# Performance work log

Measured on AMD Instinct MI355X. Metric: run time of the kernel, lower is better.

## Reference

```python
import jax, jax.numpy as jnp
import numpy as np

NUM_HEADS = 16
HIDDEN = 1024
HEAD_DIM = HIDDEN // NUM_HEADS
B, S, D = 2, 2048, 1024


def setup_inputs() -> dict:
    key = jax.random.key(0)
    ks = jax.random.split(key, 7)
    scale = 1.0 / np.sqrt(D)
    return {
        "query": jax.random.normal(ks[0], (B, S, D), dtype=jnp.float32),
        "key": jax.random.normal(ks[1], (B, S, D), dtype=jnp.float32),
        "value": jax.random.normal(ks[2], (B, S, D), dtype=jnp.float32),
        "Wk_w": jax.random.normal(ks[3], (HIDDEN, D), dtype=jnp.float32) * scale,
        "Wk_b": jax.random.normal(ks[4], (HIDDEN,), dtype=jnp.float32) * scale,
        "Wv_w": jax.random.normal(ks[5], (HIDDEN, D), dtype=jnp.float32) * scale,
        "Wv_b": jax.random.normal(ks[6], (HIDDEN,), dtype=jnp.float32) * scale,
    }


def reference(query, key, value, Wk_w, Wk_b, Wv_w, Wv_b):
    # NOTE: in the original torch module, self.W_v is assigned twice, so the
    # SAME Linear (Wv) projects both key and value; Wk projects query.
    b, s, _ = query.shape

    def split_heads(x):  # [b,s,hidden] -> [b,h,s,hd]
        return x.reshape(b, s, NUM_HEADS, HEAD_DIM).transpose(0, 2, 1, 3)

    q = split_heads(query @ Wk_w.T + Wk_b)
    k = split_heads(key @ Wv_w.T + Wv_b)
    v = split_heads(value @ Wv_w.T + Wv_b)

    scores = jnp.einsum("bhqd,bhkd->bhqk", q, k) / jnp.sqrt(
        jnp.asarray(HEAD_DIM, dtype=q.dtype))
    probs = jax.nn.softmax(scores, axis=-1)
    out = jnp.einsum("bhqk,bhkd->bhqd", probs, v)
    return out.transpose(0, 2, 1, 3).reshape(b, s, NUM_HEADS * HEAD_DIM)
```

## Files before the change

kernel.cpp:

```cpp
#include <hip/hip_runtime.h>
#include <stdint.h>

typedef unsigned short u16;
typedef uint32_t u32;
typedef __bf16 bf16x8 __attribute__((ext_vector_type(8)));
typedef float f32x4 __attribute__((ext_vector_type(4)));
typedef u16 u16x4 __attribute__((ext_vector_type(4)));
typedef u16 u16x8 __attribute__((ext_vector_type(8)));

#define XQ_OFF 0ul
#define XK_OFF 4194304ul
#define XV_OFF 8388608ul
#define WK_OFF 12582912ul
#define WV_OFF 13631488ul
#define Q_OFF  14680064ul
#define K_OFF  18874368ul
#define V_OFF  23068672ul

#define SCQ 0.18033688011112042f

#if __has_builtin(__builtin_amdgcn_exp2f)
#define EXP2F(x) __builtin_amdgcn_exp2f(x)
#else
#define EXP2F(x) exp2f(x)
#endif

__device__ __forceinline__ u16 f2bf(float f) {
  u32 u = __float_as_uint(f);
  u32 r = (u + 0x7fffu + ((u >> 16) & 1u)) >> 16;
  return (u16)r;
}

__device__ __forceinline__ u32 pk2(float a, float b) {
  typedef __bf16 bf2_t __attribute__((ext_vector_type(2)));
  typedef float f2_t __attribute__((ext_vector_type(2)));
  f2_t v; v[0] = a; v[1] = b;
  bf2_t h = __builtin_convertvector(v, bf2_t);
  union { bf2_t h; u32 u; } cv; cv.h = h; return cv.u;
}

__device__ __forceinline__ void load_lds16(const void* g, void* l) {
  __builtin_amdgcn_global_load_lds(
      (const __attribute__((address_space(1))) u32*)g,
      (__attribute__((address_space(3))) u32*)l, 16, 0, 0);
}

__device__ __forceinline__ u32 swz(u32 L) {
  return L ^ (((L >> 7) & 1u) << 4) ^ (((L >> 10) & 3u) << 5);
}

__global__ __launch_bounds__(256) void cvt_tile_kernel(
    const float* __restrict__ xq, const float* __restrict__ xk,
    const float* __restrict__ xv, const float* __restrict__ wk,
    const float* __restrict__ wv, u16* __restrict__ ws) {
  __shared__ u16 tile[4096];
  const int bid = blockIdx.x;
  const float* src; size_t dstbase; int rt, ktp;
  if (bid < 3072) {
    int m = bid >> 10, loc = bid & 1023;
    src = (m == 0) ? xq : (m == 1) ? xk : xv;
    dstbase = (size_t)m * 4194304ul;
    rt = loc >> 4; ktp = loc & 15;
  } else {
    int r2 = bid - 3072;
    int m = r2 >> 8, loc = r2 & 255;
    src = m ? wv : wk;
    dstbase = WK_OFF + (size_t)m * 1048576ul;
    rt = loc >> 4; ktp = loc & 15;
  }
  const int t = threadIdx.x;
  const int row0 = t >> 4, c = t & 15;
  const int k = c * 4;
  const float* s = src + (size_t)(rt * 64 + row0) * 1024ul + ktp * 64 + k;
#pragma unroll
  for (int i = 0; i < 4; ++i) {
    float4 v = *(const float4*)(s + (size_t)i * 16384ul);
    int row = row0 + i * 16;
    u32* p = (u32*)(tile + ((k >> 5) * 2048 + ((k >> 3) & 3) * 512 + row * 8 + (k & 7)));
    p[0] = pk2(v.x, v.y);
    p[1] = pk2(v.z, v.w);
  }
  __syncthreads();
  u16* dst = ws + dstbase + (size_t)(rt * 32 + ktp * 2) * 2048ul;
#pragma unroll
  for (int so = 0; so < 4096; so += 2048)
    *(u16x8*)(dst + so + t * 8) = *(const u16x8*)(tile + so + t * 8);
}

__global__ __launch_bounds__(256, 3) void proj_kernel(u16* __restrict__ ws,
                                                      const float* __restrict__ bk,
                                                      const float* __restrict__ bv) {
  const int proj = blockIdx.z;
  const int mtile = blockIdx.x;
  const int ntile = blockIdx.y;
  const u16* A = ws + (size_t)proj * 4194304ul;
  const u16* Bw = ws + ((proj == 0) ? WK_OFF : WV_OFF);
  const float* bias = (proj == 0) ? bk : bv;
  u16* outQ = ws + Q_OFF;
  u16* outK = ws + K_OFF;
  u16* outV = ws + V_OFF;

  const int t = threadIdx.x;
  const int w = t >> 6, lane = t & 63;
  const int wm = w >> 1, wn = w & 1;
  const int g = lane >> 4, c = lane & 15;

  __shared__ __align__(16) u16 As[2][2][2048];
  __shared__ __align__(16) u16 Bs[2][2][2048];

  const u16* Ag = A + (size_t)(2 * mtile) * 65536ul;
  const u16* Bg = Bw + (size_t)(2 * ntile) * 65536ul;
  const u32 t8 = (u32)t * 8u;
  const u32 so = swz((u32)t * 16u) >> 1;

  u32 poff[4];
#pragma unroll
  for (int mt = 0; mt < 4; ++mt)
    poff[mt] = swz((u32)((g << 10) | ((mt * 16 + c) << 4))) >> 1;

#define PSTAGE(buf, kt)                                            \
  do {                                                             \
    const size_t ko = (size_t)(kt) * 2048ul + so;                  \
    load_lds16(Ag + ko, &As[buf][0][t8]);                          \
    load_lds16(Ag + 65536ul + ko, &As[buf][1][t8]);                \
    load_lds16(Bg + ko, &Bs[buf][0][t8]);                          \
    load_lds16(Bg + 65536ul + ko, &Bs[buf][1][t8]);                \
  } while (0)

  f32x4 acc[4][4];
#pragma unroll
  for (int mt = 0; mt < 4; ++mt)
#pragma unroll
    for (int nt = 0; nt < 4; ++nt) acc[mt][nt] = (f32x4){0.f, 0.f, 0.f, 0.f};

  PSTAGE(0, 0);
  __syncthreads();

#pragma unroll 1
  for (int kt = 0; kt < 32; ++kt) {
    const int cur = kt & 1;
    if (kt < 31) PSTAGE(cur ^ 1, kt + 1);
    const u16* Ap = As[cur][wm];
    const u16* Bp = Bs[cur][wn];
    bf16x8 af[4], bfv[4];
#pragma unroll
    for (int mt = 0; mt < 4; ++mt) af[mt] = *(const bf16x8*)(Ap + poff[mt]);
#pragma unroll
    for (int nt = 0; nt < 4; ++nt) bfv[nt] = *(const bf16x8*)(Bp + poff[nt]);
#pragma unroll
    for (int mt = 0; mt < 4; ++mt)
#pragma unroll
      for (int nt = 0; nt < 4; ++nt)
        acc[mt][nt] =
            __builtin_amdgcn_mfma_f32_16x16x32_bf16(af[mt], bfv[nt], acc[mt][nt], 0, 0, 0);
    __syncthreads();
  }
#undef PSTAGE

  const int m0 = mtile * 128 + wm * 64;
  const int n0 = ntile * 128 + wn * 64;
#pragma unroll
  for (int nt = 0; nt < 4; ++nt) {
    const int col = n0 + nt * 16 + c;
    const float bvv = bias[col];
    const int h = col >> 6, d = col & 63;
#pragma unroll
    for (int mt = 0; mt < 4; ++mt) {
      const int mbase = m0 + mt * 16 + g * 4;
      const int b = mbase >> 11;
      const int bh = b * 16 + h;
      const int s = mbase & 2047;
      if (proj == 2) {
        u16x4 pk;
#pragma unroll
        for (int r = 0; r < 4; ++r) pk[r] = f2bf(acc[mt][nt][r] + bvv);
        size_t idx = (size_t)bh * 131072ul + (size_t)(s >> 6) * 4096ul +
                     (size_t)((s & 63) >> 3) * 512ul + (size_t)d * 8ul + (size_t)(s & 7);
        *(u16x4*)(outV + idx) = pk;
      } else {
        u16* dst = (proj == 0) ? outQ : outK;
#pragma unroll
        for (int r = 0; r < 4; ++r) {
          const int m = mbase + r;
          const int s2 = m & 2047;
          float y = acc[mt][nt][r] + bvv;
          if (proj == 0) y *= SCQ;
          size_t idx;
          if (proj == 0)
            idx = (size_t)bh * 131072ul + (size_t)(s2 >> 7) * 8192ul + (size_t)(d >> 3) * 1024ul +
                  (size_t)(s2 & 127) * 8ul + (size_t)(d & 7);
          else
            idx = (size_t)bh * 131072ul + (size_t)(s2 >> 6) * 4096ul + (size_t)(d >> 3) * 512ul +
                  (size_t)(s2 & 63) * 8ul + (size_t)(d & 7);
          dst[idx] = f2bf(y);
        }
      }
    }
  }
}

__device__ __forceinline__ void attn_step(
    int jj, const u16* __restrict__ Kg, const u16* __restrict__ Vg,
    bf16x8 (&kf)[2][4], bf16x8 (&vcur)[2][4], bf16x8 (&vnxt)[2][4],
    const bf16x8 (&qf)[2][2], const bf16x8 onesf, f32x4 (&O)[2][4],
    f32x4 (&Lacc)[2], u16* __restrict__ Psw, int g, int c) {
  const int jn = (jj < 31) ? jj + 1 : 31;
  const u16* Vn = Vg + (size_t)jn * 4096ul;
#pragma unroll
  for (int ksh = 0; ksh < 2; ++ksh)
#pragma unroll
    for (int nt = 0; nt < 4; ++nt)
      vnxt[ksh][nt] = *(const bf16x8*)(Vn + (ksh * 4 + g) * 512 + (nt * 16 + c) * 8);

  f32x4 St[4][2];
#pragma unroll
  for (int mtk = 0; mtk < 4; ++mtk)
#pragma unroll
    for (int ntq = 0; ntq < 2; ++ntq) St[mtk][ntq] = (f32x4){0.f, 0.f, 0.f, 0.f};
  __builtin_amdgcn_s_setprio(1);
#pragma unroll
  for (int ks = 0; ks < 2; ++ks)
#pragma unroll
    for (int mtk = 0; mtk < 4; ++mtk)
#pragma unroll
      for (int ntq = 0; ntq < 2; ++ntq)
        St[mtk][ntq] =
            __builtin_amdgcn_mfma_f32_16x16x32_bf16(kf[ks][mtk], qf[ntq][ks], St[mtk][ntq], 0, 0, 0);
  __builtin_amdgcn_s_setprio(0);

  const u16* Kn = Kg + (size_t)jn * 4096ul;
#pragma unroll
  for (int ks = 0; ks < 2; ++ks)
#pragma unroll
    for (int mtk = 0; mtk < 4; ++mtk)
      kf[ks][mtk] = *(const bf16x8*)(Kn + (ks * 4 + g) * 512 + (mtk * 16 + c) * 8);

#pragma unroll
  for (int mtk = 0; mtk < 4; ++mtk)
#pragma unroll
    for (int ntq = 0; ntq < 2; ++ntq)
#pragma unroll
      for (int r = 0; r < 4; ++r) St[mtk][ntq][r] = EXP2F(St[mtk][ntq][r]);

#pragma unroll
  for (int ksh = 0; ksh < 2; ++ksh) {
#pragma unroll
    for (int ntq = 0; ntq < 2; ++ntq)
#pragma unroll
      for (int m2 = 0; m2 < 2; ++m2) {
        const int mtk = ksh * 2 + m2;
        u32 lo = pk2(St[mtk][ntq][0], St[mtk][ntq][1]);
        u32 hi = pk2(St[mtk][ntq][2], St[mtk][ntq][3]);
        u32* p = (u32*)(Psw + (ntq * 16 + c) * 40 + m2 * 16 + g * 4);
        p[0] = lo; p[1] = hi;
      }
    asm volatile("s_waitcnt lgkmcnt(0)" ::: "memory");
    bf16x8 pf[2];
#pragma unroll
    for (int mtq = 0; mtq < 2; ++mtq)
      pf[mtq] = *(const bf16x8*)(Psw + (mtq * 16 + c) * 40 + g * 8);
    __builtin_amdgcn_s_setprio(1);
#pragma unroll
    for (int mtq = 0; mtq < 2; ++mtq) {
      Lacc[mtq] = __builtin_amdgcn_mfma_f32_16x16x32_bf16(pf[mtq], onesf, Lacc[mtq], 0, 0, 0);
#pragma unroll
      for (int nt = 0; nt < 4; ++nt)
        O[mtq][nt] =
            __builtin_amdgcn_mfma_f32_16x16x32_bf16(pf[mtq], vcur[ksh][nt], O[mtq][nt], 0, 0, 0);
    }
    __builtin_amdgcn_s_setprio(0);
  }
}

__global__ __launch_bounds__(256, 2) void attn_kernel(const u16* __restrict__ ws,
                                                      float* __restrict__ out) {
  const int bh = blockIdx.x, qtile = blockIdx.y;
  const int b = bh >> 4, h = bh & 15;
  const int t = threadIdx.x, w = t >> 6, lane = t & 63, g = lane >> 4, c = lane & 15;

  __shared__ __align__(16) u16 Ps[4][1280];

  const u16* Qg = ws + Q_OFF + (size_t)bh * 131072ul + (size_t)qtile * 8192ul;
  const u16* Kg = ws + K_OFF + (size_t)bh * 131072ul;
  const u16* Vg = ws + V_OFF + (size_t)bh * 131072ul;

  bf16x8 qf[2][2];
#pragma unroll
  for (int ntq = 0; ntq < 2; ++ntq)
#pragma unroll
    for (int ks = 0; ks < 2; ++ks)
      qf[ntq][ks] = *(const bf16x8*)(Qg + (ks * 4 + g) * 1024 + (w * 32 + ntq * 16 + c) * 8);

  u16x8 ou;
#pragma unroll
  for (int i = 0; i < 8; ++i) ou[i] = (u16)0x3F80;
  union { u16x8 u; bf16x8 b; } ocv; ocv.u = ou;
  const bf16x8 onesf = ocv.b;

  f32x4 O[2][4], Lacc[2];
#pragma unroll
  for (int mtq = 0; mtq < 2; ++mtq) {
    Lacc[mtq] = (f32x4){0.f, 0.f, 0.f, 0.f};
#pragma unroll
    for (int nt = 0; nt < 4; ++nt) O[mtq][nt] = (f32x4){0.f, 0.f, 0.f, 0.f};
  }

  u16* Psw = Ps[w];

  bf16x8 kf[2][4];
#pragma unroll
  for (int ks = 0; ks < 2; ++ks)
#pragma unroll
    for (int mtk = 0; mtk < 4; ++mtk)
      kf[ks][mtk] = *(const bf16x8*)(Kg + (ks * 4 + g) * 512 + (mtk * 16 + c) * 8);
  bf16x8 vfA[2][4], vfB[2][4];
#pragma unroll
  for (int ksh = 0; ksh < 2; ++ksh)
#pragma unroll
    for (int nt = 0; nt < 4; ++nt)
      vfA[ksh][nt] = *(const bf16x8*)(Vg + (ksh * 4 + g) * 512 + (nt * 16 + c) * 8);

#pragma unroll 1
  for (int j2 = 0; j2 < 16; ++j2) {
    attn_step(2 * j2, Kg, Vg, kf, vfA, vfB, qf, onesf, O, Lacc, Psw, g, c);
    attn_step(2 * j2 + 1, Kg, Vg, kf, vfB, vfA, qf, onesf, O, Lacc, Psw, g, c);
  }

  const int q0 = qtile * 128 + w * 32;
#pragma unroll
  for (int mtq = 0; mtq < 2; ++mtq)
#pragma unroll
    for (int r = 0; r < 4; ++r) {
      const float inv = 1.0f / Lacc[mtq][r];
      const int q = q0 + mtq * 16 + g * 4 + r;
      float* rowp = out + (size_t)(b * 2048 + q) * 1024ul + h * 64;
#pragma unroll
      for (int nt = 0; nt < 4; ++nt) rowp[nt * 16 + c] = O[mtq][nt][r] * inv;
    }
}

extern "C" void kernel_launch(void* const* d_in, const int* in_sizes, int n_in,
                              void* d_out, int out_size, void* d_ws, size_t ws_size,
                              hipStream_t stream) {
  const float* q = (const float*)d_in[0];
  const float* k = (const float*)d_in[1];
  const float* v = (const float*)d_in[2];
  const float* wk = (const float*)d_in[3];
  const float* bk = (const float*)d_in[4];
  const float* wv = (const float*)d_in[5];
  const float* bv = (const float*)d_in[6];
  u16* ws = (u16*)d_ws;
  float* out = (float*)d_out;

  cvt_tile_kernel<<<3584, 256, 0, stream>>>(q, k, v, wk, wv, ws);
  proj_kernel<<<dim3(32, 8, 3), 256, 0, stream>>>(ws, bk, bv);
  attn_kernel<<<dim3(32, 16), 256, 0, stream>>>(ws, out);
}
```

Baseline: 180.3 us.

## Triple-buffer projection GEMM loads and stage Q/K epilogue through LDS

The projection GEMM moves from a double-buffered LDS pipeline to a three-stage ring. It prefetches two k-tiles ahead and uses an explicit vmcnt wait plus s_barrier in place of a full __syncthreads per iteration. The Q/K epilogue now writes bf16 results into per-warp LDS tiles first, then stores them to global memory as coalesced 16-byte vectors, replacing scattered 2-byte stores. This raises LDS use to 48KB per block, which may lower occupancy, and relies on hand-counted vmcnt values being correct.

```diff
diff --git a/kernel.cpp b/kernel.cpp
--- a/kernel.cpp
+++ b/kernel.cpp
@@ -105,8 +105,7 @@
   const int wm = w >> 1, wn = w & 1;
   const int g = lane >> 4, c = lane & 15;
 
-  __shared__ __align__(16) u16 As[2][2][2048];
-  __shared__ __align__(16) u16 Bs[2][2][2048];
+  __shared__ __align__(16) u16 smem[24576];
 
   const u16* Ag = A + (size_t)(2 * mtile) * 65536ul;
   const u16* Bg = Bw + (size_t)(2 * ntile) * 65536ul;
@@ -120,13 +119,29 @@
 
 #define PSTAGE(buf, kt)                                            \
   do {                                                             \
+    u16* bb = smem + (buf) * 8192;                                 \
     const size_t ko = (size_t)(kt) * 2048ul + so;                  \
-    load_lds16(Ag + ko, &As[buf][0][t8]);                          \
-    load_lds16(Ag + 65536ul + ko, &As[buf][1][t8]);                \
-    load_lds16(Bg + ko, &Bs[buf][0][t8]);                          \
-    load_lds16(Bg + 65536ul + ko, &Bs[buf][1][t8]);                \
+    load_lds16(Ag + ko, bb + t8);                                  \
+    load_lds16(Ag + 65536ul + ko, bb + 2048 + t8);                 \
+    load_lds16(Bg + ko, bb + 4096 + t8);                           \
+    load_lds16(Bg + 65536ul + ko, bb + 6144 + t8);                 \
   } while (0)
 
+#define PFRAGS_MFMA(buf)                                                        \
+  do {                                                                          \
+    const u16* Ap = smem + (buf) * 8192 + wm * 2048;                            \
+    const u16* Bp = smem + (buf) * 8192 + 4096 + wn * 2048;                     \
+    bf16x8 af[4], bfv[4];                                                       \
+    _Pragma("unroll") for (int mt = 0; mt < 4; ++mt)                            \
+        af[mt] = *(const bf16x8*)(Ap + poff[mt]);                               \
+    _Pragma("unroll") for (int nt = 0; nt < 4; ++nt)                            \
+        bfv[nt] = *(const bf16x8*)(Bp + poff[nt]);                              \
+    _Pragma("unroll") for (int mt = 0; mt < 4; ++mt)                            \
+        _Pragma("unroll") for (int nt = 0; nt < 4; ++nt)                        \
+            acc[mt][nt] = __builtin_amdgcn_mfma_f32_16x16x32_bf16(              \
+                af[mt], bfv[nt], acc[mt][nt], 0, 0, 0);                         \
+  } while (0)
+
   f32x4 acc[4][4];
 #pragma unroll
   for (int mt = 0; mt < 4; ++mt)
@@ -134,67 +149,75 @@
     for (int nt = 0; nt < 4; ++nt) acc[mt][nt] = (f32x4){0.f, 0.f, 0.f, 0.f};
 
   PSTAGE(0, 0);
-  __syncthreads();
-
+  PSTAGE(1, 1);
+
+  int cur = 0, stg = 2;
 #pragma unroll 1
-  for (int kt = 0; kt < 32; ++kt) {
-    const int cur = kt & 1;
-    if (kt < 31) PSTAGE(cur ^ 1, kt + 1);
-    const u16* Ap = As[cur][wm];
-    const u16* Bp = Bs[cur][wn];
-    bf16x8 af[4], bfv[4];
-#pragma unroll
-    for (int mt = 0; mt < 4; ++mt) af[mt] = *(const bf16x8*)(Ap + poff[mt]);
-#pragma unroll
-    for (int nt = 0; nt < 4; ++nt) bfv[nt] = *(const bf16x8*)(Bp + poff[nt]);
-#pragma unroll
-    for (int mt = 0; mt < 4; ++mt)
-#pragma unroll
-      for (int nt = 0; nt < 4; ++nt)
-        acc[mt][nt] =
-            __builtin_amdgcn_mfma_f32_16x16x32_bf16(af[mt], bfv[nt], acc[mt][nt], 0, 0, 0);
-    __syncthreads();
-  }
+  for (int kt = 0; kt < 31; ++kt) {
+    asm volatile("s_waitcnt vmcnt(4)\n\ts_barrier" ::: "memory");
+    if (kt < 30) PSTAGE(stg, kt + 2);
+    PFRAGS_MFMA(cur);
+    cur = (cur == 2) ? 0 : cur + 1;
+    stg = (stg == 2) ? 0 : stg + 1;
+  }
+  asm volatile("s_waitcnt vmcnt(0)\n\ts_barrier" ::: "memory");
+  PFRAGS_MFMA(cur);
 #undef PSTAGE
+#undef PFRAGS_MFMA
 
   const int m0 = mtile * 128 + wm * 64;
   const int n0 = ntile * 128 + wn * 64;
-#pragma unroll
-  for (int nt = 0; nt < 4; ++nt) {
-    const int col = n0 + nt * 16 + c;
-    const float bvv = bias[col];
-    const int h = col >> 6, d = col & 63;
-#pragma unroll
-    for (int mt = 0; mt < 4; ++mt) {
-      const int mbase = m0 + mt * 16 + g * 4;
-      const int b = mbase >> 11;
-      const int bh = b * 16 + h;
-      const int s = mbase & 2047;
-      if (proj == 2) {
+  if (proj == 2) {
+#pragma unroll
+    for (int nt = 0; nt < 4; ++nt) {
+      const int col = n0 + nt * 16 + c;
+      const float bvv = bias[col];
+      const int h = col >> 6, d = col & 63;
+#pragma unroll
+      for (int mt = 0; mt < 4; ++mt) {
+        const int mbase = m0 + mt * 16 + g * 4;
+        const int b = mbase >> 11;
+        const int bh = b * 16 + h;
+        const int s = mbase & 2047;
         u16x4 pk;
 #pragma unroll
         for (int r = 0; r < 4; ++r) pk[r] = f2bf(acc[mt][nt][r] + bvv);
         size_t idx = (size_t)bh * 131072ul + (size_t)(s >> 6) * 4096ul +
                      (size_t)((s & 63) >> 3) * 512ul + (size_t)d * 8ul + (size_t)(s & 7);
         *(u16x4*)(outV + idx) = pk;
-      } else {
-        u16* dst = (proj == 0) ? outQ : outK;
+      }
+    }
+  } else {
+    __syncthreads();
+    u16* Ew = smem + w * 4096;
+#pragma unroll
+    for (int nt = 0; nt < 4; ++nt) {
+      const int d = nt * 16 + c;
+      const float bvv = bias[n0 + nt * 16 + c];
+#pragma unroll
+      for (int mt = 0; mt < 4; ++mt) {
 #pragma unroll
         for (int r = 0; r < 4; ++r) {
-          const int m = mbase + r;
-          const int s2 = m & 2047;
+          const int srow = mt * 16 + g * 4 + r;
           float y = acc[mt][nt][r] + bvv;
           if (proj == 0) y *= SCQ;
-          size_t idx;
-          if (proj == 0)
-            idx = (size_t)bh * 131072ul + (size_t)(s2 >> 7) * 8192ul + (size_t)(d >> 3) * 1024ul +
-                  (size_t)(s2 & 127) * 8ul + (size_t)(d & 7);
-          else
-            idx = (size_t)bh * 131072ul + (size_t)(s2 >> 6) * 4096ul + (size_t)(d >> 3) * 512ul +
-                  (size_t)(s2 & 63) * 8ul + (size_t)(d & 7);
-          dst[idx] = f2bf(y);
+          Ew[(d >> 3) * 512 + srow * 8 + (d & 7)] = f2bf(y);
         }
       }
+    }
+    __syncthreads();
+    const int b = mtile >> 4;
+    const int bh = b * 16 + ntile * 2 + wn;
+    if (proj == 0) {
+      u16* base = outQ + (size_t)bh * 131072ul + (size_t)(mtile & 15) * 8192ul + wm * 512;
+#pragma unroll
+      for (int i = 0; i < 8; ++i)
+        *(u16x8*)(base + i * 1024 + lane * 8) = *(const u16x8*)(Ew + i * 512 + lane * 8);
+    } else {
+      u16* base = outK + (size_t)bh * 131072ul + (size_t)((mtile & 15) * 2 + wm) * 4096ul;
+#pragma unroll
+      for (int i = 0; i < 8; ++i)
+        *(u16x8*)(base + i * 512 + lane * 8) = *(const u16x8*)(Ew + i * 512 + lane * 8);
     }
   }
 }
```

Measured after the change: 175.5 us. 1.03x faster.
